# Kernel optimization log

Hardware: AMD Instinct MI355X
Metric: run time of the kernel (lower is better)

Reference implementation:

```python
import jax, jax.numpy as jnp
import numpy as np

FP4_E2M1_VALUES = [0.0, 0.0625, 8.0, 1.0, 2.0, 3.0, 4.0, 6.0,
                   -0.0, -0.0625, -8.0, -1.0, -2.0, -3.0, -4.0, -6.0]

M, N, K = 4096, 4096, 4096


def setup_inputs() -> dict:
    key = jax.random.key(0)
    k1, k2 = jax.random.split(key)
    x = jax.random.normal(k1, (M, K), dtype=jnp.float16)
    # packed uint8 bytes stored as int32 (values in [0,256)); each byte holds
    # two fp4 indices: high nibble = even k, low nibble = odd k
    packed_weight = jax.random.randint(k2, (N, K // 2), 0, 256, dtype=jnp.int32)
    lut = jnp.array(FP4_E2M1_VALUES, dtype=jnp.float16)
    return {"x": x, "packed_weight": packed_weight, "lut": lut}


def reference(x, packed_weight, lut):
    # Dequantize: unpack nibbles along K, LUT lookup -> W [N, K] fp16
    n, kh = packed_weight.shape
    high = (packed_weight >> 4) & 15   # even k positions
    low = packed_weight & 15           # odd k positions
    idx = jnp.stack([high, low], axis=-1).reshape(n, 2 * kh)  # [N, K]
    w = lut[idx]                       # [N, K] fp16
    # GEMM with fp32 accumulation (Triton kernel accumulates in fp32), cast to fp16
    y = jnp.einsum('mk,nk->mn', x, w, preferred_element_type=jnp.float32)
    return y.astype(jnp.float16)
```

## Files before the change

### kernel.cpp

```cpp
#include <hip/hip_runtime.h>
#include <hip/hip_fp16.h>
#include <stdint.h>

#define M_DIM 4096
#define N_DIM 4096
#define K_DIM 4096
#define KW (K_DIM / 2)
#define WS_XH_BYTES ((size_t)M_DIM * K_DIM * 2)
#define WS_WH_BYTES ((size_t)N_DIM * K_DIM * 2)

typedef _Float16 half8 __attribute__((ext_vector_type(8)));
typedef float f32x4 __attribute__((ext_vector_type(4)));

__device__ __forceinline__ uint32_t pk2(float a, float b) {
  auto h = __builtin_amdgcn_cvt_pkrtz(a, b);
  return __builtin_bit_cast(uint32_t, h);
}

__device__ __forceinline__ uint32_t dq(uint32_t b, uint32_t ph, uint32_t pl) {
#if __has_builtin(__builtin_amdgcn_perm)
  const uint32_t sel = ((b & 0x70u) << 4) | ((b & 0x07u) << 24);
  uint32_t v = __builtin_amdgcn_perm(ph, pl, sel);
#else
  const uint64_t pool = ((uint64_t)ph << 32) | pl;
  const uint32_t mh = (uint32_t)(pool >> (((b >> 4) & 7u) * 8)) & 0xFFu;
  const uint32_t ml = (uint32_t)(pool >> ((b & 7u) * 8)) & 0xFFu;
  uint32_t v = (mh << 8) | (ml << 24);
#endif
  const uint32_t sg = ((b & 0x88u) * 0x10000100u) & 0x80008000u;
  return v | sg;
}

__device__ __forceinline__ void lut_pool(const float* __restrict__ lutf,
                                         uint32_t& ph, uint32_t& pl) {
  const uint32_t h01 = pk2(lutf[0], lutf[1]);
  const uint32_t h23 = pk2(lutf[2], lutf[3]);
  const uint32_t h45 = pk2(lutf[4], lutf[5]);
  const uint32_t h67 = pk2(lutf[6], lutf[7]);
#if __has_builtin(__builtin_amdgcn_perm)
  pl = __builtin_amdgcn_perm(h23, h01, 0x07050301u);
  ph = __builtin_amdgcn_perm(h67, h45, 0x07050301u);
#else
  pl = ((h01 >> 8) & 0xFFu) | ((h01 >> 24) << 8) |
       (((h23 >> 8) & 0xFFu) << 16) | ((h23 >> 24) << 24);
  ph = ((h45 >> 8) & 0xFFu) | ((h45 >> 24) << 8) |
       (((h67 >> 8) & 0xFFu) << 16) | ((h67 >> 24) << 24);
#endif
}

#define XBLOCKS (M_DIM * K_DIM / 8 / 256)
#define WBLOCKS (N_DIM * KW / 4 / 256)

__global__ __launch_bounds__(256) void prep_kernel(
    const float4* __restrict__ xin, uint4* __restrict__ xout,
    const int4* __restrict__ pin, uint4* __restrict__ wout,
    const float* __restrict__ lutf) {
  const int b = blockIdx.x;
  if (b < XBLOCKS) {
    const int i = b * 256 + threadIdx.x;
    const float4 v0 = xin[2 * i];
    const float4 v1 = xin[2 * i + 1];
    xout[i] = make_uint4(pk2(v0.x, v0.y), pk2(v0.z, v0.w),
                         pk2(v1.x, v1.y), pk2(v1.z, v1.w));
  } else {
    uint32_t ph, pl;
    lut_pool(lutf, ph, pl);
    const int i = (b - XBLOCKS) * 256 + threadIdx.x;
    const int4 w = pin[i];
    wout[i] = make_uint4(dq(w.x, ph, pl), dq(w.y, ph, pl),
                         dq(w.z, ph, pl), dq(w.w, ph, pl));
  }
}

__global__ __launch_bounds__(256) void cvt_x_kernel(const float4* __restrict__ xin,
                                                    uint4* __restrict__ xout) {
  const int i = blockIdx.x * 256 + threadIdx.x;
  const float4 v0 = xin[2 * i];
  const float4 v1 = xin[2 * i + 1];
  xout[i] = make_uint4(pk2(v0.x, v0.y), pk2(v0.z, v0.w),
                       pk2(v1.x, v1.y), pk2(v1.z, v1.w));
}

__device__ __forceinline__ f32x4 mfma16(half8 a, half8 b, f32x4 c) {
  return __builtin_amdgcn_mfma_f32_16x16x32_f16(a, b, c, 0, 0, 0);
}

#define NT (K_DIM / 64)
#define SGB __builtin_amdgcn_sched_group_barrier
#define SG_MFMA 0x8
#define SG_DSRD 0x100

__global__ __launch_bounds__(512, 2) void f16gemm256_kernel(
    const uint8_t* __restrict__ xh,
    const uint8_t* __restrict__ wh,
    float* __restrict__ out)
{
  __shared__ uint16_t Al[2][2][256 * 32];
  __shared__ uint16_t Bl[2][2][256 * 32];

  const int tid  = threadIdx.x;
  const int lane = tid & 63;
  const int wave = tid >> 6;
  const int wm   = wave >> 2;
  const int wn   = wave & 3;

  const int bid = blockIdx.x;
  const int sw  = (bid & 7) * 32 + (bid >> 3);
  const int m0  = (sw >> 4) * 256;
  const int n0  = (sw & 15) * 256;

  const uint8_t* asrc[2];
  const uint8_t* bsrc[2];
  int ldst[2];
#pragma unroll
  for (int s = 0; s < 2; ++s) {
    const int slot = tid + s * 512;
    const int row  = slot >> 2;
    const int g    = (slot & 3) ^ ((row >> 1) & 3);
    asrc[s] = xh + ((size_t)(m0 + row) * K_DIM) * 2 + g * 16;
    bsrc[s] = wh + ((size_t)(n0 + row) * K_DIM) * 2 + g * 16;
    ldst[s] = slot * 16;
  }

  auto STAGE = [&](int isB, int buf, int kh, int tt) {
    const int koff  = tt * 128 + kh * 64;
    uint8_t* lb = (uint8_t*)(isB ? &Bl[0][0][0] : &Al[0][0][0]) +
                  (buf * 2 + kh) * 16384;
#pragma unroll
    for (int s = 0; s < 2; ++s) {
      const uint8_t* gp = (isB ? bsrc[s] : asrc[s]) + koff;
      __builtin_amdgcn_global_load_lds(
          (const __attribute__((address_space(1))) uint32_t*)gp,
          (__attribute__((address_space(3))) uint32_t*)(lb + ldst[s]), 16, 0, 0);
    }
  };

  int aoff[8], boff[4];
#pragma unroll
  for (int m = 0; m < 8; ++m) {
    const int row = wm * 128 + m * 16 + (lane & 15);
    const int ch  = (lane >> 4) ^ ((row >> 1) & 3);
    aoff[m] = row * 32 + ch * 8;
  }
#pragma unroll
  for (int n = 0; n < 4; ++n) {
    const int row = wn * 64 + n * 16 + (lane & 15);
    const int ch  = (lane >> 4) ^ ((row >> 1) & 3);
    boff[n] = row * 32 + ch * 8;
  }

  f32x4 acc[8][4];
#pragma unroll
  for (int i = 0; i < 8; ++i)
#pragma unroll
    for (int j = 0; j < 4; ++j) acc[i][j] = (f32x4){0.f, 0.f, 0.f, 0.f};

  STAGE(1, 0, 0, 0);
  STAGE(0, 0, 0, 0);
  STAGE(1, 0, 1, 0);
  STAGE(0, 0, 1, 0);
  STAGE(1, 1, 0, 1);
  STAGE(0, 1, 0, 1);
  asm volatile("s_waitcnt vmcnt(8)" ::: "memory");
  __builtin_amdgcn_s_barrier();

  half8 af[8], bfr[4];

#pragma unroll 2
  for (int t = 0; t < NT; ++t) {
    const int cur = t & 1;
    const uint16_t* Ab = &Al[cur][0][0];
    const uint16_t* Bb = &Bl[cur][0][0];
    const bool st1 = (t + 1 < NT);
    const bool st2 = (t + 2 < NT);

    __builtin_amdgcn_s_setprio(1);
    bfr[0] = *(const half8*)(Bb + boff[0]);
    bfr[1] = *(const half8*)(Bb + boff[1]);
    bfr[2] = *(const half8*)(Bb + boff[2]);
    bfr[3] = *(const half8*)(Bb + boff[3]);
    af[0] = *(const half8*)(Ab + aoff[0]);
    af[1] = *(const half8*)(Ab + aoff[1]);
    SGB(SG_DSRD, 6, 0);
    if (st1) { STAGE(1, cur ^ 1, 1, t + 1); STAGE(0, cur ^ 1, 1, t + 1); }
#pragma unroll
    for (int m = 0; m < 8; ++m) {
      if (m + 2 < 8) {
        af[m + 2] = *(const half8*)(Ab + aoff[m + 2]);
        SGB(SG_DSRD, 1, 0);
      }
      acc[m][0] = mfma16(af[m], bfr[0], acc[m][0]);
      acc[m][1] = mfma16(af[m], bfr[1], acc[m][1]);
      acc[m][2] = mfma16(af[m], bfr[2], acc[m][2]);
      acc[m][3] = mfma16(af[m], bfr[3], acc[m][3]);
      SGB(SG_MFMA, 4, 0);
    }
    __builtin_amdgcn_s_setprio(0);
    if (st1) asm volatile("s_waitcnt vmcnt(8)" ::: "memory");
    else     asm volatile("s_waitcnt vmcnt(0)" ::: "memory");
    __builtin_amdgcn_s_barrier();

    __builtin_amdgcn_s_setprio(1);
    bfr[0] = *(const half8*)(Bb + 8192 + boff[0]);
    bfr[1] = *(const half8*)(Bb + 8192 + boff[1]);
    bfr[2] = *(const half8*)(Bb + 8192 + boff[2]);
    bfr[3] = *(const half8*)(Bb + 8192 + boff[3]);
    af[0] = *(const half8*)(Ab + 8192 + aoff[0]);
    af[1] = *(const half8*)(Ab + 8192 + aoff[1]);
    SGB(SG_DSRD, 6, 0);
    if (st2) { STAGE(1, cur, 0, t + 2); STAGE(0, cur, 0, t + 2); }
#pragma unroll
    for (int m = 0; m < 8; ++m) {
      if (m + 2 < 8) {
        af[m + 2] = *(const half8*)(Ab + 8192 + aoff[m + 2]);
        SGB(SG_DSRD, 1, 0);
      }
      acc[m][0] = mfma16(af[m], bfr[0], acc[m][0]);
      acc[m][1] = mfma16(af[m], bfr[1], acc[m][1]);
      acc[m][2] = mfma16(af[m], bfr[2], acc[m][2]);
      acc[m][3] = mfma16(af[m], bfr[3], acc[m][3]);
      SGB(SG_MFMA, 4, 0);
    }
    __builtin_amdgcn_s_setprio(0);
    if (st2)      asm volatile("s_waitcnt vmcnt(8)" ::: "memory");
    else if (st1) asm volatile("s_waitcnt vmcnt(4)" ::: "memory");
    __builtin_amdgcn_s_barrier();
  }

  const int mb = m0 + wm * 128 + (lane >> 4) * 4;
  const int nb = n0 + wn * 64 + (lane & 15);
#pragma unroll
  for (int m = 0; m < 8; ++m)
#pragma unroll
    for (int n = 0; n < 4; ++n)
#pragma unroll
      for (int r = 0; r < 4; ++r)
        out[(size_t)(mb + m * 16 + r) * N_DIM + (nb + n * 16)] = acc[m][n][r];
}

#define BM 128
#define BN 128
#define BK 32

__global__ __launch_bounds__(256, 2) void fp4gemm_kernel(
    const uint8_t* __restrict__ xh, const int* __restrict__ pw,
    const float* __restrict__ lutf, float* __restrict__ out)
{
  __shared__ uint16_t ldsA[BM * BK];
  __shared__ uint16_t ldsB[BN * BK];

  const int tid  = threadIdx.x;
  const int lane = tid & 63;
  const int wave = tid >> 6;
  const int wm   = wave >> 1;
  const int wn   = wave & 1;
  const int m0 = blockIdx.y * BM;
  const int n0 = blockIdx.x * BN;

  uint32_t ph, pl;
  lut_pool(lutf, ph, pl);

  f32x4 acc[4][4];
#pragma unroll
  for (int i = 0; i < 4; ++i)
#pragma unroll
    for (int j = 0; j < 4; ++j) acc[i][j] = (f32x4){0.f, 0.f, 0.f, 0.f};

  const int rowB  = tid >> 1;
  const int halfB = tid & 1;
  const int swzB  = (rowB >> 1) & 3;

  for (int kt = 0; kt < K_DIM / BK; ++kt) {
    __syncthreads();

#pragma unroll
    for (int s = 0; s < 2; ++s) {
      const int idx = tid + s * 256;
      const int row = idx >> 2;
      const int c16 = idx & 3;
      const int g16 = c16 ^ ((row >> 1) & 3);
      const uint8_t* gp = xh + ((size_t)(m0 + row) * K_DIM + kt * BK) * 2 + g16 * 16;
      uint8_t* lp = (uint8_t*)ldsA + (size_t)idx * 16;
      __builtin_amdgcn_global_load_lds(
          (const __attribute__((address_space(1))) uint32_t*)gp,
          (__attribute__((address_space(3))) uint32_t*)lp, 16, 0, 0);
    }

    {
      const int* gp = pw + (size_t)(n0 + rowB) * KW + kt * (BK / 2) + halfB * 8;
      const int4 wA = ((const int4*)gp)[0];
      const int4 wB = ((const int4*)gp)[1];
      uint8_t* base = (uint8_t*)ldsB + rowB * 64;
      *(uint4*)(base + ((halfB * 2 + 0) ^ swzB) * 16) =
          make_uint4(dq(wA.x, ph, pl), dq(wA.y, ph, pl),
                     dq(wA.z, ph, pl), dq(wA.w, ph, pl));
      *(uint4*)(base + ((halfB * 2 + 1) ^ swzB) * 16) =
          make_uint4(dq(wB.x, ph, pl), dq(wB.y, ph, pl),
                     dq(wB.z, ph, pl), dq(wB.w, ph, pl));
    }

    __syncthreads();

    const int q = lane >> 4;
    half8 af[4], bfr[4];
#pragma unroll
    for (int i = 0; i < 4; ++i) {
      const int row = wm * 64 + i * 16 + (lane & 15);
      af[i] = *(const half8*)(ldsA + row * BK + (q ^ ((row >> 1) & 3)) * 8);
    }
#pragma unroll
    for (int j = 0; j < 4; ++j) {
      const int row = wn * 64 + j * 16 + (lane & 15);
      bfr[j] = *(const half8*)(ldsB + row * BK + (q ^ ((row >> 1) & 3)) * 8);
    }
#pragma unroll
    for (int i = 0; i < 4; ++i)
#pragma unroll
      for (int j = 0; j < 4; ++j)
        acc[i][j] = __builtin_amdgcn_mfma_f32_16x16x32_f16(af[i], bfr[j], acc[i][j], 0, 0, 0);
  }

  const int mb = m0 + wm * 64 + (lane >> 4) * 4;
  const int nb = n0 + wn * 64 + (lane & 15);
#pragma unroll
  for (int i = 0; i < 4; ++i)
#pragma unroll
    for (int j = 0; j < 4; ++j)
#pragma unroll
      for (int r = 0; r < 4; ++r)
        out[(size_t)(mb + i * 16 + r) * N_DIM + (nb + j * 16)] = acc[i][j][r];
}

extern "C" void kernel_launch(void* const* d_in, const int* in_sizes, int n_in,
                              void* d_out, int out_size, void* d_ws, size_t ws_size,
                              hipStream_t stream) {
  const void* px = nullptr; const void* ppw = nullptr; const void* plut = nullptr;
  for (int i = 0; i < n_in; ++i) {
    const long s = in_sizes[i];
    if (s == (long)M_DIM * K_DIM) px = d_in[i];
    else if (s == (long)N_DIM * KW) ppw = d_in[i];
    else if (s == 16) plut = d_in[i];
  }
  if (!px || !ppw || !plut) { px = d_in[0]; ppw = d_in[1]; plut = d_in[2]; }

  if (ws_size >= WS_XH_BYTES + WS_WH_BYTES) {
    uint8_t* wh = (uint8_t*)d_ws + WS_XH_BYTES;
    prep_kernel<<<XBLOCKS + WBLOCKS, 256, 0, stream>>>(
        (const float4*)px, (uint4*)d_ws, (const int4*)ppw, (uint4*)wh,
        (const float*)plut);
    f16gemm256_kernel<<<dim3(256), dim3(512), 0, stream>>>(
        (const uint8_t*)d_ws, wh, (float*)d_out);
  } else {
    cvt_x_kernel<<<(M_DIM * K_DIM / 8) / 256, 256, 0, stream>>>(
        (const float4*)px, (uint4*)d_ws);
    dim3 grid(N_DIM / BN, M_DIM / BM);
    fp4gemm_kernel<<<grid, dim3(256), 0, stream>>>(
        (const uint8_t*)d_ws, (const int*)ppw, (const float*)plut, (float*)d_out);
  }
}
```

Before: 253.4 us.

## Restructure K-loop to one barrier per tile with full-tile prefetch

```diff
diff --git a/kernel.cpp b/kernel.cpp
--- a/kernel.cpp
+++ b/kernel.cpp
@@ -88,6 +88,7 @@
 #define NT (K_DIM / 64)
 #define SGB __builtin_amdgcn_sched_group_barrier
 #define SG_MFMA 0x8
+#define SG_VMEM 0x10
 #define SG_DSRD 0x100
 
 __global__ __launch_bounds__(512, 2) void f16gemm256_kernel(
@@ -159,9 +160,7 @@
   STAGE(0, 0, 0, 0);
   STAGE(1, 0, 1, 0);
   STAGE(0, 0, 1, 0);
-  STAGE(1, 1, 0, 1);
-  STAGE(0, 1, 0, 1);
-  asm volatile("s_waitcnt vmcnt(8)" ::: "memory");
+  asm volatile("s_waitcnt vmcnt(0)" ::: "memory");
   __builtin_amdgcn_s_barrier();
 
   half8 af[8], bfr[4];
@@ -172,58 +171,60 @@
     const uint16_t* Ab = &Al[cur][0][0];
     const uint16_t* Bb = &Bl[cur][0][0];
     const bool st1 = (t + 1 < NT);
-    const bool st2 = (t + 2 < NT);
 
     __builtin_amdgcn_s_setprio(1);
+
     bfr[0] = *(const half8*)(Bb + boff[0]);
     bfr[1] = *(const half8*)(Bb + boff[1]);
     bfr[2] = *(const half8*)(Bb + boff[2]);
     bfr[3] = *(const half8*)(Bb + boff[3]);
     af[0] = *(const half8*)(Ab + aoff[0]);
     af[1] = *(const half8*)(Ab + aoff[1]);
-    SGB(SG_DSRD, 6, 0);
-    if (st1) { STAGE(1, cur ^ 1, 1, t + 1); STAGE(0, cur ^ 1, 1, t + 1); }
+
+    if (st1) {
+      STAGE(1, cur ^ 1, 0, t + 1);
+      STAGE(0, cur ^ 1, 0, t + 1);
+      STAGE(1, cur ^ 1, 1, t + 1);
+      STAGE(0, cur ^ 1, 1, t + 1);
+    }
+
+#pragma unroll
+    for (int m = 2; m < 8; ++m) af[m] = *(const half8*)(Ab + aoff[m]);
+
 #pragma unroll
     for (int m = 0; m < 8; ++m) {
-      if (m + 2 < 8) {
-        af[m + 2] = *(const half8*)(Ab + aoff[m + 2]);
-        SGB(SG_DSRD, 1, 0);
-      }
       acc[m][0] = mfma16(af[m], bfr[0], acc[m][0]);
       acc[m][1] = mfma16(af[m], bfr[1], acc[m][1]);
       acc[m][2] = mfma16(af[m], bfr[2], acc[m][2]);
       acc[m][3] = mfma16(af[m], bfr[3], acc[m][3]);
-      SGB(SG_MFMA, 4, 0);
-    }
-    __builtin_amdgcn_s_setprio(0);
-    if (st1) asm volatile("s_waitcnt vmcnt(8)" ::: "memory");
-    else     asm volatile("s_waitcnt vmcnt(0)" ::: "memory");
-    __builtin_amdgcn_s_barrier();
-
-    __builtin_amdgcn_s_setprio(1);
+    }
+
     bfr[0] = *(const half8*)(Bb + 8192 + boff[0]);
     bfr[1] = *(const half8*)(Bb + 8192 + boff[1]);
     bfr[2] = *(const half8*)(Bb + 8192 + boff[2]);
     bfr[3] = *(const half8*)(Bb + 8192 + boff[3]);
-    af[0] = *(const half8*)(Ab + 8192 + aoff[0]);
-    af[1] = *(const half8*)(Ab + 8192 + aoff[1]);
-    SGB(SG_DSRD, 6, 0);
-    if (st2) { STAGE(1, cur, 0, t + 2); STAGE(0, cur, 0, t + 2); }
+#pragma unroll
+    for (int m = 0; m < 8; ++m) af[m] = *(const half8*)(Ab + 8192 + aoff[m]);
+
 #pragma unroll
     for (int m = 0; m < 8; ++m) {
-      if (m + 2 < 8) {
-        af[m + 2] = *(const half8*)(Ab + 8192 + aoff[m + 2]);
-        SGB(SG_DSRD, 1, 0);
-      }
       acc[m][0] = mfma16(af[m], bfr[0], acc[m][0]);
       acc[m][1] = mfma16(af[m], bfr[1], acc[m][1]);
       acc[m][2] = mfma16(af[m], bfr[2], acc[m][2]);
       acc[m][3] = mfma16(af[m], bfr[3], acc[m][3]);
-      SGB(SG_MFMA, 4, 0);
-    }
+    }
+
+    SGB(SG_DSRD, 6, 0);
+    SGB(SG_VMEM, 8, 0);
+#pragma unroll
+    for (int i = 0; i < 18; ++i) {
+      SGB(SG_MFMA, 2, 0);
+      SGB(SG_DSRD, 1, 0);
+    }
+    SGB(SG_MFMA, 28, 0);
+
     __builtin_amdgcn_s_setprio(0);
-    if (st2)      asm volatile("s_waitcnt vmcnt(8)" ::: "memory");
-    else if (st1) asm volatile("s_waitcnt vmcnt(4)" ::: "memory");
+    if (st1) asm volatile("s_waitcnt vmcnt(0)" ::: "memory");
     __builtin_amdgcn_s_barrier();
   }
 
```

Result: slower. 258.9 us (+2.2%).
